# Kernel tuning notes

Measured on AMD Instinct MI355X. Metric: run time of the kernel, lower is better.

## Reference

```python
import jax, jax.numpy as jnp
import numpy as np

H = 16
DH = 64
THETA = 10000.0


def setup_inputs() -> dict:
    key = jax.random.key(0)
    ks = jax.random.split(key, 9)
    B, M, R = 4, 1024, 256
    d = H * DH
    s = 0.05
    return {
        "Pq": jax.random.normal(ks[0], (B, M, R), jnp.float32) * s,
        "Pk": jax.random.normal(ks[1], (B, M, R), jnp.float32) * s,
        "Pv": jax.random.normal(ks[2], (B, M, R), jnp.float32) * s,
        "Vq": jax.random.normal(ks[3], (R, d), jnp.float32) * s,
        "Vk": jax.random.normal(ks[4], (R, d), jnp.float32) * s,
        "Vv": jax.random.normal(ks[5], (R, d), jnp.float32) * s,
        "bq": jax.random.normal(ks[6], (d,), jnp.float32) * s,
        "bk": jax.random.normal(ks[7], (d,), jnp.float32) * s,
        "bv": jax.random.normal(ks[8], (d,), jnp.float32) * s,
        "attention_mask": jnp.ones((B, M), jnp.int32),
        "position_ids": jnp.tile(jnp.arange(M, dtype=jnp.int32), (B, 1)),
    }


def _rope_cos_sin(position_ids):
    # half-dim frequencies, matching the kernel's half-half rotation
    half = DH // 2
    inv_freq = 1.0 / (THETA ** (jnp.arange(0, half, dtype=jnp.float32) / half))
    ang = position_ids.astype(jnp.float32)[..., None] * inv_freq  # [B,M,half]
    return jnp.cos(ang), jnp.sin(ang)


def _rotate(x, cos, sin):
    # x: [B,H,M,dh]; cos/sin: [B,M,half] -> broadcast over heads
    half = DH // 2
    x0, x1 = x[..., :half], x[..., half:]
    c = cos[:, None, :, :]
    s = sin[:, None, :, :]
    return jnp.concatenate([x0 * c - x1 * s, x0 * s + x1 * c], axis=-1)


def reference(Pq, Pk, Pv, Vq, Vk, Vv, bq, bk, bv, attention_mask, position_ids):
    B, M, R = Pq.shape
    # reconstruct per-head Q/K/V from low-rank factors
    Vq3 = Vq.reshape(R, H, DH)
    Vk3 = Vk.reshape(R, H, DH)
    Vv3 = Vv.reshape(R, H, DH)
    q = jnp.einsum("bmr,rhd->bhmd", Pq, Vq3) + bq.reshape(H, DH)[None, :, None, :]
    k = jnp.einsum("bmr,rhd->bhmd", Pk, Vk3) + bk.reshape(H, DH)[None, :, None, :]
    v = jnp.einsum("bmr,rhd->bhmd", Pv, Vv3) + bv.reshape(H, DH)[None, :, None, :]
    cos, sin = _rope_cos_sin(position_ids)
    q = _rotate(q, cos, sin)
    k = _rotate(k, cos, sin)
    scale = 1.0 / jnp.sqrt(jnp.float32(DH))
    scores = jnp.einsum("bhmd,bhnd->bhmn", q, k) * scale  # [B,H,M,M]
    valid = attention_mask.astype(bool)
    pad = valid[:, None, :, None] & valid[:, None, None, :]
    scores = jnp.where(pad, scores, -jnp.inf)
    p = jax.nn.softmax(scores, axis=-1)
    out = jnp.einsum("bhmn,bhnd->bhmd", p, v)
    return out
```

## Files before the change

kernel.cpp:

```cpp
#include <hip/hip_runtime.h>
#include <hip/hip_bf16.h>
#include <math.h>

#define BB 4
#define MM 1024
#define RR 256
#define HH 16
#define DHH 64
#define DD (HH*DHH)

typedef __attribute__((ext_vector_type(8))) short short8;
typedef __attribute__((ext_vector_type(4))) float f32x4;

static __device__ __forceinline__ unsigned short f2bf(float x) {
    __hip_bfloat16 h = __float2bfloat16(x);
    return *(unsigned short*)&h;
}

#if defined(__has_builtin)
#  if __has_builtin(__builtin_amdgcn_exp2f)
#    define EXP2F(x) __builtin_amdgcn_exp2f(x)
#  endif
#endif
#ifndef EXP2F
#  define EXP2F(x) __expf((x) * 0.6931471805599453f)
#endif

static __device__ __forceinline__ unsigned pack_bf16_rh(float a, float b) {
    unsigned ua = __builtin_bit_cast(unsigned, a) + 0x8000u;
    unsigned ub = __builtin_bit_cast(unsigned, b) + 0x8000u;
    return __builtin_amdgcn_perm(ub, ua, 0x07060302u);
}

static __device__ __forceinline__ void gload_lds16(const void* g, void* l) {
    __builtin_amdgcn_global_load_lds(
        (const __attribute__((address_space(1))) unsigned int*)g,
        (__attribute__((address_space(3))) unsigned int*)l, 16, 0, 0);
}

__global__ __launch_bounds__(256) void prep_kernel(
    const float* __restrict__ Pq, const float* __restrict__ Pk, const float* __restrict__ Pv,
    const float* __restrict__ Vq, const float* __restrict__ Vk, const float* __restrict__ Vv,
    __hip_bfloat16* __restrict__ VTq, __hip_bfloat16* __restrict__ VTk,
    __hip_bfloat16* __restrict__ VTv, __hip_bfloat16* __restrict__ Pb)
{
    const int t = threadIdx.x;
    if (blockIdx.x < 768) {
        const int z   = blockIdx.x / 256;
        const int rem = blockIdx.x % 256;
        const int r0  = (rem & 7) * 32;
        const int d0  = (rem >> 3) * 32;
        const float* V = (z == 0) ? Vq : (z == 1) ? Vk : Vv;
        __hip_bfloat16* VT = (z == 0) ? VTq : (z == 1) ? VTk : VTv;

        __shared__ __hip_bfloat16 Ts[32][33];
        {
            const int row = t >> 3;
            const int c4  = (t & 7) * 4;
            float4 f = *(const float4*)&V[(size_t)(r0 + row) * DD + d0 + c4];
            Ts[row][c4 + 0] = __float2bfloat16(f.x);
            Ts[row][c4 + 1] = __float2bfloat16(f.y);
            Ts[row][c4 + 2] = __float2bfloat16(f.z);
            Ts[row][c4 + 3] = __float2bfloat16(f.w);
        }
        __syncthreads();
        {
            const int orow = t >> 3;
            const int oc4  = (t & 7) * 4;
            union { unsigned short u[4]; uint2 v; } pk;
            #pragma unroll
            for (int i = 0; i < 4; ++i) pk.u[i] = *(unsigned short*)&Ts[oc4 + i][orow];
            *(uint2*)&VT[(size_t)(d0 + orow) * RR + r0 + oc4] = pk.v;
        }
    } else {
        const size_t n4 = (size_t)BB * MM * RR / 4;
        size_t i = (size_t)(blockIdx.x - 768) * 256 + t;
        const int which = (int)(i / n4);
        const size_t off = i - (size_t)which * n4;
        const float* P = (which == 0) ? Pq : (which == 1) ? Pk : Pv;
        float4 f = *(const float4*)(P + off * 4);
        union { unsigned short u[4]; uint2 v; } pk;
        pk.u[0] = f2bf(f.x); pk.u[1] = f2bf(f.y); pk.u[2] = f2bf(f.z); pk.u[3] = f2bf(f.w);
        *(uint2*)((unsigned short*)Pb + (size_t)which * BB * MM * RR + off * 4) = pk.v;
    }
}

__global__ __launch_bounds__(256) void svd_gemm(
    const __hip_bfloat16* __restrict__ Pb,
    const __hip_bfloat16* __restrict__ VTq, const __hip_bfloat16* __restrict__ VTk,
    const __hip_bfloat16* __restrict__ VTv,
    const float* __restrict__ bq, const float* __restrict__ bk, const float* __restrict__ bv,
    const int* __restrict__ pos_ids,
    __hip_bfloat16* __restrict__ qout, __hip_bfloat16* __restrict__ kout,
    __hip_bfloat16* __restrict__ vTout)
{
    const int which = blockIdx.z;
    const short* P = (const short*)Pb + (size_t)which * BB * MM * RR;
    const __hip_bfloat16* VT = (which == 0) ? VTq : (which == 1) ? VTk : VTv;
    const float* bias        = (which == 0) ? bq : (which == 1) ? bk : bv;

    const int h   = blockIdx.y;
    const int bm0 = blockIdx.x * 256;
    const int b   = bm0 >> 10;
    const int m0  = bm0 & 1023;
    const int tid = threadIdx.x;
    const int lane = tid & 63;
    const int w    = tid >> 6;
    const int l15  = lane & 15;
    const int quad = lane >> 4;

    __shared__ alignas(16) short SM[256 * 72 + 64 * 72];
    short* As = SM;
    short* Bs = SM + 256 * 72;

    f32x4 acc[4][4];
    #pragma unroll
    for (int mt = 0; mt < 4; ++mt)
        #pragma unroll
        for (int dt = 0; dt < 4; ++dt) acc[mt][dt] = (f32x4){0.f, 0.f, 0.f, 0.f};

    for (int kc = 0; kc < 4; ++kc) {
        #pragma unroll
        for (int i = 0; i < 8; ++i) {
            int u = tid + i * 256;
            int row = u >> 3;
            int cg  = (u & 7) * 8;
            *(uint4*)&As[row * 72 + cg] =
                *(const uint4*)&P[(size_t)(bm0 + row) * RR + kc * 64 + cg];
        }
        #pragma unroll
        for (int i = 0; i < 2; ++i) {
            int u = tid + i * 256;
            int row = u >> 3;
            int cg  = (u & 7) * 8;
            *(uint4*)&Bs[row * 72 + cg] =
                *(const uint4*)((const short*)VT + (size_t)(h * 64 + row) * RR + kc * 64 + cg);
        }
        __syncthreads();

        #pragma unroll
        for (int ks = 0; ks < 2; ++ks) {
            short8 a[4];
            #pragma unroll
            for (int mt = 0; mt < 4; ++mt)
                a[mt] = *(const short8*)&As[(w * 64 + mt * 16 + l15) * 72 + ks * 32 + quad * 8];
            #pragma unroll
            for (int dt = 0; dt < 4; ++dt) {
                short8 bf = *(const short8*)&Bs[(dt * 16 + l15) * 72 + ks * 32 + quad * 8];
                #pragma unroll
                for (int mt = 0; mt < 4; ++mt)
                    acc[mt][dt] = __builtin_amdgcn_mfma_f32_16x16x32_bf16(a[mt], bf, acc[mt][dt], 0, 0, 0);
            }
        }
        __syncthreads();
    }

    #pragma unroll
    for (int dt = 0; dt < 4; ++dt) {
        float bc = bias[h * 64 + dt * 16 + l15];
        #pragma unroll
        for (int mt = 0; mt < 4; ++mt)
            #pragma unroll
            for (int r = 0; r < 4; ++r) acc[mt][dt][r] += bc;
    }

    if (which < 2) {
        __hip_bfloat16* out = (which == 0) ? qout : kout;
        int pm[4][4];
        #pragma unroll
        for (int mt = 0; mt < 4; ++mt)
            #pragma unroll
            for (int r = 0; r < 4; ++r)
                pm[mt][r] = pos_ids[bm0 + w * 64 + mt * 16 + quad * 4 + r];
        float cB[2][4][4], sB[2][4][4];
        #pragma unroll
        for (int f2 = 0; f2 < 2; ++f2) {
            float invf = __powf(10000.0f, -(float)(f2 * 16 + l15) * (1.0f / 32.0f));
            #pragma unroll
            for (int mt = 0; mt < 4; ++mt)
                #pragma unroll
                for (int r = 0; r < 4; ++r) {
                    float ang = (float)pm[mt][r] * invf;
                    __sincosf(ang, &sB[f2][mt][r], &cB[f2][mt][r]);
                }
        }
        #pragma unroll
        for (int dt = 0; dt < 4; ++dt) {
            const int cd = dt * 16 + l15;
            const int f2 = dt & 1;
            #pragma unroll
            for (int mt = 0; mt < 4; ++mt)
                #pragma unroll
                for (int r = 0; r < 4; ++r) {
                    float x  = acc[mt][dt][r];
                    float xp = acc[mt][dt ^ 2][r];
                    float c = cB[f2][mt][r], s = sB[f2][mt][r];
                    float val = (dt < 2) ? (x * c - xp * s) : (xp * s + x * c);
                    int m = m0 + w * 64 + mt * 16 + quad * 4 + r;
                    out[(((size_t)b * HH + h) * MM + m) * DHH + cd] = __float2bfloat16(val);
                }
        }
    } else {
        short* Tt = SM;
        __syncthreads();
        #pragma unroll
        for (int dt = 0; dt < 4; ++dt)
            #pragma unroll
            for (int mt = 0; mt < 4; ++mt) {
                union { unsigned short u[4]; uint2 v; } pk;
                #pragma unroll
                for (int r = 0; r < 4; ++r) pk.u[r] = f2bf(acc[mt][dt][r]);
                *(uint2*)&Tt[(dt * 16 + l15) * 264 + w * 64 + mt * 16 + quad * 4] = pk.v;
            }
        __syncthreads();
        #pragma unroll
        for (int it = 0; it < 8; ++it) {
            int u = tid + it * 256;
            int row = u >> 5;
            int seg = u & 31;
            *(uint4*)&vTout[(((size_t)b * HH + h) * DHH + row) * MM + m0 + seg * 8] =
                *(const uint4*)&Tt[row * 264 + seg * 8];
        }
    }
}

__global__ __launch_bounds__(256, 2) void attn_kernel(
    const __hip_bfloat16* __restrict__ q, const __hip_bfloat16* __restrict__ k,
    const __hip_bfloat16* __restrict__ vT,
    const int* __restrict__ mask, float* __restrict__ out)
{
    const int bh   = blockIdx.x & 63;
    const int qt   = blockIdx.x >> 6;
    const int b    = bh >> 4;
    const int tid  = threadIdx.x;
    const int lane = tid & 63;
    const int w    = tid >> 6;
    const int l15  = lane & 15;
    const int quad = lane >> 4;
    const int q0   = qt * 128;

    __shared__ alignas(16) short KtL[2][128 * 64];
    __shared__ alignas(16) __hip_bfloat16 Vt[2][64][136];

    const short* kbase = (const short*)k  + (size_t)bh * MM * DHH;
    const short* vbase = (const short*)vT + (size_t)bh * DHH * MM;

    short8 qa[2][2];
    #pragma unroll
    for (int mt = 0; mt < 2; ++mt) {
        const short* qb = (const short*)q +
            ((size_t)bh * MM + q0 + w * 32 + mt * 16 + l15) * DHH + quad * 8;
        qa[mt][0] = *(const short8*)(qb);
        qa[mt][1] = *(const short8*)(qb + 32);
    }

    f32x4 Ot[2][4];
    #pragma unroll
    for (int mt = 0; mt < 2; ++mt)
        #pragma unroll
        for (int dt = 0; dt < 4; ++dt) Ot[mt][dt] = (f32x4){0.f, 0.f, 0.f, 0.f};
    float lsum[2] = {0.f, 0.f};

    const int* maskb = mask + b * MM;
    const int srcbase = (lane & 48) | ((lane & 48) >> 2);
    const float k2 = 0.125f * 1.44269504089f;

    const int p0 = quad ^ (l15 & 7);
    const int p1 = (quad + 4) ^ (l15 & 7);

    {
        #pragma unroll
        for (int pass = 0; pass < 4; ++pass) {
            int u = tid + pass * 256;
            int row = u >> 3;
            int gl  = (u & 7) ^ (row & 7);
            gload_lds16(kbase + (size_t)row * DHH + gl * 8, &KtL[0][u * 8]);
        }
        #pragma unroll
        for (int pass = 0; pass < 4; ++pass) {
            int u = tid + pass * 256;
            int row = u >> 4, c = u & 15;
            union { uint4 q4; uint2 h2[2]; } vld;
            vld.q4 = *(const uint4*)(vbase + (size_t)row * MM + c * 8);
            int g = c >> 3, c6 = c & 7;
            int base0 = g * 64 + (c6 >> 2) * 32 + (c6 & 1) * 16 + ((c6 >> 1) & 1) * 4;
            *(uint2*)&Vt[0][row][base0]     = vld.h2[0];
            *(uint2*)&Vt[0][row][base0 + 8] = vld.h2[1];
        }
        __syncthreads();
    }

    for (int nc = 0; nc < MM / 128; ++nc) {
        const int cur = nc & 1;
        const int n0  = nc * 128;

        uint4 vreg[4];
        if (nc < 7) {
            const short* vb2 = vbase + n0 + 128;
            #pragma unroll
            for (int pass = 0; pass < 4; ++pass) {
                int u = tid + pass * 256, row = u >> 4, c = u & 15;
                vreg[pass] = *(const uint4*)(vb2 + (size_t)row * MM + c * 8);
            }
            const short* kb2 = kbase + (size_t)(n0 + 128) * DHH;
            #pragma unroll
            for (int pass = 0; pass < 4; ++pass) {
                int u = tid + pass * 256;
                int row = u >> 3;
                int gl  = (u & 7) ^ (row & 7);
                gload_lds16(kb2 + (size_t)row * DHH + gl * 8, &KtL[cur ^ 1][u * 8]);
            }
        }

        unsigned long long bal0 = __ballot(maskb[n0 + lane] != 0);
        unsigned long long bal1 = __ballot(maskb[n0 + 64 + lane] != 0);

        f32x4 S[2][8];
        __builtin_amdgcn_s_setprio(1);
        #pragma unroll
        for (int t = 0; t < 8; ++t) {
            const short* krow = &KtL[cur][(t * 16 + l15) * 64];
            short8 ka0 = *(const short8*)(krow + p0 * 8);
            short8 ka1 = *(const short8*)(krow + p1 * 8);
            #pragma unroll
            for (int mt = 0; mt < 2; ++mt) {
                f32x4 c = (f32x4){0.f, 0.f, 0.f, 0.f};
                c = __builtin_amdgcn_mfma_f32_16x16x32_bf16(ka0, qa[mt][0], c, 0, 0, 0);
                c = __builtin_amdgcn_mfma_f32_16x16x32_bf16(ka1, qa[mt][1], c, 0, 0, 0);
                S[mt][t] = c;
            }
        }
        __builtin_amdgcn_s_setprio(0);

        #pragma unroll
        for (int t = 0; t < 8; ++t) {
            unsigned bits = (unsigned)((t < 4 ? bal0 : bal1) >> ((t & 3) * 16 + quad * 4));
            #pragma unroll
            for (int r = 0; r < 4; ++r) {
                float sb = ((bits >> r) & 1u) ? 0.0f : -1e30f;
                #pragma unroll
                for (int mt = 0; mt < 2; ++mt) {
                    float e = EXP2F(fmaf(S[mt][t][r], k2, sb));
                    lsum[mt] += e;
                    S[mt][t][r] = e;
                }
            }
        }

        short8 pa[2][4];
        #pragma unroll
        for (int mt = 0; mt < 2; ++mt)
            #pragma unroll
            for (int p = 0; p < 4; ++p) {
                union { unsigned u[4]; short8 s; } pk;
                pk.u[0] = pack_bf16_rh(S[mt][2*p][0],   S[mt][2*p][1]);
                pk.u[1] = pack_bf16_rh(S[mt][2*p][2],   S[mt][2*p][3]);
                pk.u[2] = pack_bf16_rh(S[mt][2*p+1][0], S[mt][2*p+1][1]);
                pk.u[3] = pack_bf16_rh(S[mt][2*p+1][2], S[mt][2*p+1][3]);
                pa[mt][p] = pk.s;
            }

        __builtin_amdgcn_s_setprio(1);
        #pragma unroll
        for (int p = 0; p < 4; ++p) {
            #pragma unroll
            for (int dt = 0; dt < 4; ++dt) {
                short8 vb = *(const short8*)&Vt[cur][dt * 16 + l15][p * 32 + quad * 8];
                #pragma unroll
                for (int mt = 0; mt < 2; ++mt)
                    Ot[mt][dt] = __builtin_amdgcn_mfma_f32_16x16x32_bf16(pa[mt][p], vb, Ot[mt][dt], 0, 0, 0);
            }
        }
        __builtin_amdgcn_s_setprio(0);

        if (nc < 7) {
            #pragma unroll
            for (int pass = 0; pass < 4; ++pass) {
                int u = tid + pass * 256, row = u >> 4, c = u & 15;
                union { uint4 q4; uint2 h2[2]; } vld;
                vld.q4 = vreg[pass];
                int g = c >> 3, c6 = c & 7;
                int base0 = g * 64 + (c6 >> 2) * 32 + (c6 & 1) * 16 + ((c6 >> 1) & 1) * 4;
                *(uint2*)&Vt[cur ^ 1][row][base0]     = vld.h2[0];
                *(uint2*)&Vt[cur ^ 1][row][base0 + 8] = vld.h2[1];
            }
        }
        __syncthreads();
    }

    #pragma unroll
    for (int mt = 0; mt < 2; ++mt) {
        float s = lsum[mt];
        s += __shfl_xor(s, 16, 64);
        s += __shfl_xor(s, 32, 64);
        float inv = 1.0f / s;
        float* ob = out + ((size_t)bh * MM + q0 + w * 32 + mt * 16) * DHH;
        #pragma unroll
        for (int r = 0; r < 4; ++r) {
            float ir = __shfl(inv, srcbase + r, 64);
            #pragma unroll
            for (int dt = 0; dt < 4; ++dt)
                ob[(quad * 4 + r) * DHH + dt * 16 + l15] = Ot[mt][dt][r] * ir;
        }
    }
}

extern "C" void kernel_launch(void* const* d_in, const int* in_sizes, int n_in,
                              void* d_out, int out_size, void* d_ws, size_t ws_size,
                              hipStream_t stream) {
    const float* Pq = (const float*)d_in[0];
    const float* Pk = (const float*)d_in[1];
    const float* Pv = (const float*)d_in[2];
    const float* Vq = (const float*)d_in[3];
    const float* Vk = (const float*)d_in[4];
    const float* Vv = (const float*)d_in[5];
    const float* bq = (const float*)d_in[6];
    const float* bk = (const float*)d_in[7];
    const float* bv = (const float*)d_in[8];
    const int* mask = (const int*)d_in[9];
    const int* pos  = (const int*)d_in[10];
    float* out = (float*)d_out;

    const size_t qkv_elems = (size_t)BB * HH * MM * DHH;
    __hip_bfloat16* qb  = (__hip_bfloat16*)d_ws;
    __hip_bfloat16* kb  = qb + qkv_elems;
    __hip_bfloat16* vT  = kb + qkv_elems;
    __hip_bfloat16* VTq = vT + qkv_elems;
    __hip_bfloat16* VTk = VTq + (size_t)DD * RR;
    __hip_bfloat16* VTv = VTk + (size_t)DD * RR;
    __hip_bfloat16* Pb  = VTv + (size_t)DD * RR;

    prep_kernel<<<768 + 3 * BB * MM * RR / 4 / 256, 256, 0, stream>>>(
        Pq, Pk, Pv, Vq, Vk, Vv, VTq, VTk, VTv, Pb);

    dim3 gG(BB * MM / 256, HH, 3);
    svd_gemm<<<gG, 256, 0, stream>>>(Pb, VTq, VTk, VTv, bq, bk, bv, pos, qb, kb, vT);

    attn_kernel<<<BB * HH * (MM / 128), 256, 0, stream>>>(qb, kb, vT, mask, out);
}
```

Baseline: 131.5 us.

## Compute softmax row sums via MFMA with ones and skip mask bias when unmasked

```diff
diff --git a/kernel.cpp b/kernel.cpp
--- a/kernel.cpp
+++ b/kernel.cpp
@@ -254,15 +254,20 @@
         qa[mt][1] = *(const short8*)(qb + 32);
     }
 
+    short8 onesB;
+    #pragma unroll
+    for (int i = 0; i < 8; ++i) onesB[i] = (short)0x3F80;
+
     f32x4 Ot[2][4];
-    #pragma unroll
-    for (int mt = 0; mt < 2; ++mt)
+    f32x4 Lacc[2];
+    #pragma unroll
+    for (int mt = 0; mt < 2; ++mt) {
         #pragma unroll
         for (int dt = 0; dt < 4; ++dt) Ot[mt][dt] = (f32x4){0.f, 0.f, 0.f, 0.f};
-    float lsum[2] = {0.f, 0.f};
+        Lacc[mt] = (f32x4){0.f, 0.f, 0.f, 0.f};
+    }
 
     const int* maskb = mask + b * MM;
-    const int srcbase = (lane & 48) | ((lane & 48) >> 2);
     const float k2 = 0.125f * 1.44269504089f;
 
     const int p0 = quad ^ (l15 & 7);
@@ -332,17 +337,24 @@
         }
         __builtin_amdgcn_s_setprio(0);
 
-        #pragma unroll
-        for (int t = 0; t < 8; ++t) {
-            unsigned bits = (unsigned)((t < 4 ? bal0 : bal1) >> ((t & 3) * 16 + quad * 4));
-            #pragma unroll
-            for (int r = 0; r < 4; ++r) {
-                float sb = ((bits >> r) & 1u) ? 0.0f : -1e30f;
-                #pragma unroll
-                for (int mt = 0; mt < 2; ++mt) {
-                    float e = EXP2F(fmaf(S[mt][t][r], k2, sb));
-                    lsum[mt] += e;
-                    S[mt][t][r] = e;
+        if ((bal0 & bal1) == ~0ull) {
+            #pragma unroll
+            for (int t = 0; t < 8; ++t)
+                #pragma unroll
+                for (int r = 0; r < 4; ++r)
+                    #pragma unroll
+                    for (int mt = 0; mt < 2; ++mt)
+                        S[mt][t][r] = EXP2F(S[mt][t][r] * k2);
+        } else {
+            #pragma unroll
+            for (int t = 0; t < 8; ++t) {
+                unsigned bits = (unsigned)((t < 4 ? bal0 : bal1) >> ((t & 3) * 16 + quad * 4));
+                #pragma unroll
+                for (int r = 0; r < 4; ++r) {
+                    float sb = ((bits >> r) & 1u) ? 0.0f : -1e30f;
+                    #pragma unroll
+                    for (int mt = 0; mt < 2; ++mt)
+                        S[mt][t][r] = EXP2F(fmaf(S[mt][t][r], k2, sb));
                 }
             }
         }
@@ -370,6 +382,9 @@
                 for (int mt = 0; mt < 2; ++mt)
                     Ot[mt][dt] = __builtin_amdgcn_mfma_f32_16x16x32_bf16(pa[mt][p], vb, Ot[mt][dt], 0, 0, 0);
             }
+            #pragma unroll
+            for (int mt = 0; mt < 2; ++mt)
+                Lacc[mt] = __builtin_amdgcn_mfma_f32_16x16x32_bf16(pa[mt][p], onesB, Lacc[mt], 0, 0, 0);
         }
         __builtin_amdgcn_s_setprio(0);
 
@@ -390,14 +405,10 @@
 
     #pragma unroll
     for (int mt = 0; mt < 2; ++mt) {
-        float s = lsum[mt];
-        s += __shfl_xor(s, 16, 64);
-        s += __shfl_xor(s, 32, 64);
-        float inv = 1.0f / s;
         float* ob = out + ((size_t)bh * MM + q0 + w * 32 + mt * 16) * DHH;
         #pragma unroll
         for (int r = 0; r < 4; ++r) {
-            float ir = __shfl(inv, srcbase + r, 64);
+            float ir = 1.0f / Lacc[mt][r];
             #pragma unroll
             for (int dt = 0; dt < 4; ++dt)
                 ob[(quad * 4 + r) * DHH + dt * 16 + l15] = Ot[mt][dt][r] * ir;
```

Result: no change. 129.1 us, median of 2 (-1.8%).
